# Performance work log

Measured on AMD Instinct MI355X. Metric: run time of the kernel, lower is better.

Reference implementation:

```python
import jax, jax.numpy as jnp
import numpy as np

H_DIM = 512
FF_DIM = 2048
N_HEAD = 4
N_BLOCK = 3
N_TOKEN = 128
B, S = 8, 1024
LN_EPS = 1e-5


def _layernorm(x, g, b):
    mu = jnp.mean(x, axis=-1, keepdims=True)
    var = jnp.mean(jnp.square(x - mu), axis=-1, keepdims=True)
    return (x - mu) * jax.lax.rsqrt(var + LN_EPS) * g + b


def setup_inputs() -> dict:
    key = jax.random.key(0)
    ks = jax.random.split(key, 20)
    sc = 0.02
    inp = {
        'input_ids': jax.random.randint(ks[0], (B, S), 0, N_TOKEN, dtype=jnp.int32),
        'attention_mask': jnp.ones((B, S), dtype=jnp.int32),
        'emb': jax.random.uniform(ks[1], (N_TOKEN, H_DIM), dtype=jnp.float32),
        'wq': jax.random.normal(ks[2], (N_BLOCK, N_HEAD, H_DIM, H_DIM), dtype=jnp.float32) * sc,
        'wk': jax.random.normal(ks[3], (N_BLOCK, N_HEAD, H_DIM, H_DIM), dtype=jnp.float32) * sc,
        'wv': jax.random.normal(ks[4], (N_BLOCK, N_HEAD, H_DIM, H_DIM), dtype=jnp.float32) * sc,
        'wo_w': jax.random.normal(ks[5], (N_BLOCK, N_HEAD * H_DIM, H_DIM), dtype=jnp.float32) * sc,
        'wo_b': jnp.zeros((N_BLOCK, H_DIM), dtype=jnp.float32),
        'ln1_g': jnp.ones((N_BLOCK, H_DIM), dtype=jnp.float32),
        'ln1_b': jnp.zeros((N_BLOCK, H_DIM), dtype=jnp.float32),
        'ff1_w': jax.random.normal(ks[6], (N_BLOCK, FF_DIM, H_DIM), dtype=jnp.float32) * sc,
        'ff1_b': jnp.zeros((N_BLOCK, FF_DIM), dtype=jnp.float32),
        'ff2_w': jax.random.normal(ks[7], (N_BLOCK, H_DIM, FF_DIM), dtype=jnp.float32) * sc,
        'ff2_b': jnp.zeros((N_BLOCK, H_DIM), dtype=jnp.float32),
        'ln2_g': jnp.ones((N_BLOCK, H_DIM), dtype=jnp.float32),
        'ln2_b': jnp.zeros((N_BLOCK, H_DIM), dtype=jnp.float32),
        'lm_w': jax.random.normal(ks[8], (H_DIM, N_TOKEN), dtype=jnp.float32) * sc,
    }
    return inp


def reference(emb, wq, wk, wv, wo_w, wo_b, ln1_g, ln1_b, ff1_w, ff1_b,
              ff2_w, ff2_b, ln2_g, ln2_b, lm_w, input_ids, attention_mask):
    mask_f = attention_mask.astype(jnp.float32)          # [B,S]
    valid = attention_mask != 0                          # [B,S]

    # Embedding lookup
    x = emb[input_ids]                                   # [B,S,H]

    # Positional encoding: positions assigned sequentially to valid tokens;
    # both even and odd feature slots get the SAME sin value (per source).
    pos = jnp.cumsum(mask_f, axis=-1) - 1.0              # [B,S]
    div = jnp.exp(jnp.arange(0, H_DIM, 2, dtype=jnp.float32) * (-jnp.log(10000.0) / H_DIM))  # [H/2]
    s = jnp.sin(pos[..., None] * div)                    # [B,S,H/2]
    pos_enc = jnp.repeat(s, 2, axis=-1) * mask_f[..., None]
    x = x + pos_enc

    # Allowed attention: causal (key <= query) AND query valid AND key valid
    rows = jnp.arange(S)
    causal = rows[None, :, None] >= rows[None, None, :]  # [1,S,S] (query>=key)
    allowed = causal & valid[:, :, None] & valid[:, None, :]  # [B,S,S]
    neg_inf = jnp.float32(-jnp.inf)
    scale = jnp.sqrt(jnp.float32(H_DIM))

    for l in range(N_BLOCK):
        # Per-head full-width attention (each head uses full H_DIM)
        q = jnp.einsum('bsh,nhd->bnsd', x, wq[l])
        k = jnp.einsum('bsh,nhd->bnsd', x, wk[l])
        v = jnp.einsum('bsh,nhd->bnsd', x, wv[l])
        scores = jnp.einsum('bnsd,bntd->bnst', q, k) / scale      # [B,N,S,S]
        scores = jnp.where(allowed[:, None], scores, neg_inf)
        att = jax.nn.softmax(scores, axis=-1)
        att = jnp.where(jnp.isnan(att), 0.0, att)                  # NaN rows -> 0
        o = jnp.einsum('bnst,bntd->bnsd', att, v)                  # [B,N,S,H]
        o = jnp.transpose(o, (0, 2, 1, 3)).reshape(B, S, N_HEAD * H_DIM)
        mh = o @ wo_w[l] + wo_b[l]
        x = _layernorm(x + mh, ln1_g[l], ln1_b[l])
        # Conv1d with kernel 1 == pointwise linear
        ff = jax.nn.relu(jnp.einsum('bsh,fh->bsf', x, ff1_w[l]) + ff1_b[l])
        ff = jnp.einsum('bsf,hf->bsh', ff, ff2_w[l]) + ff2_b[l]
        x = _layernorm(x + ff, ln2_g[l], ln2_b[l])

    return x @ lm_w                                       # [B,S,N_TOKEN]
```

## Files before the change

kernel.cpp:

```cpp
#include <hip/hip_runtime.h>
#include <hip/hip_bf16.h>

#define S_LEN 1024
#define BATCH 8
#define HD 512
#define FFD 2048
#define NHEAD 4
#define NBLK 3
#define NTOK 128

typedef __bf16 bf16_t;
typedef __bf16 bf16x4_t __attribute__((ext_vector_type(4)));
typedef __bf16 bf16x8_t __attribute__((ext_vector_type(8)));
typedef float f32x4_t __attribute__((ext_vector_type(4)));

typedef __attribute__((address_space(3))) uint32_t lds_u32;
typedef __attribute__((address_space(1))) uint32_t glb_u32;

template<int NI>
__device__ __forceinline__ void ldsread(const bf16_t* __restrict__ buf, int row0,
                                        int fr, int fg, int sw, bf16x8_t (&dst)[NI][2]) {
  #pragma unroll
  for (int i = 0; i < NI; ++i)
    #pragma unroll
    for (int ks = 0; ks < 2; ++ks)
      dst[i][ks] = *(const bf16x8_t*)&buf[(row0 + i*16 + fr)*64 + (((ks*4 + fg) ^ sw) << 3)];
}

template<int IB, int JB>
__device__ __forceinline__ void mquad(f32x4_t (&acc)[8][4],
                                      const bf16x8_t (&af)[4][2], const bf16x8_t (&bf)[2][2]) {
  #pragma unroll
  for (int ks = 0; ks < 2; ++ks)
    #pragma unroll
    for (int i = 0; i < 4; ++i)
      #pragma unroll
      for (int j = 0; j < 2; ++j)
        acc[IB+i][JB+j] = __builtin_amdgcn_mfma_f32_16x16x32_bf16(af[i][ks], bf[j][ks], acc[IB+i][JB+j], 0, 0, 0);
}

template<bool OUT_BF16, bool BIAS, bool RELU, bool CSKIP, bool CKLIM>
__global__ __launch_bounds__(512, 2)
void gemm256_kernel(const bf16_t* __restrict__ A,
                    const bf16_t* __restrict__ Bt,
                    const float* __restrict__ bias,
                    void* __restrict__ Cv,
                    int M, int N, int K,
                    int lda, int ldb, int ldc,
                    long long sA, long long sB, long long sBias,
                    int zshift, long long sC_hi, long long sC_lo,
                    int msub_shift, long long msub_stride,
                    float alpha)
{
  const int zb = blockIdx.z;
  const int m0 = blockIdx.x * 256;
  const int n0 = blockIdx.y * 256;
  if (CSKIP && n0 > m0 + 255) return;
  int kend = K;
  if (CKLIM) { int ke = m0 + 256; kend = ke < K ? ke : K; }
  const int nt = kend >> 6;

  const bf16_t* Az = A + (long long)zb * sA;
  const bf16_t* Bz = Bt + (long long)zb * sB;
  const long long coff = ((long long)(zb >> zshift)) * sC_hi
                       + ((long long)(zb & ((1 << zshift) - 1))) * sC_lo;

  __shared__ __align__(16) bf16_t As[2][256 * 64];
  __shared__ __align__(16) bf16_t Bs[2][256 * 64];

  const int tid = threadIdx.x;
  const int lane = tid & 63;
  const int w = tid >> 6;
  const int wm = (w >> 2) * 128;
  const int wn = (w & 3) * 64;
  const int fr = lane & 15;
  const int fg = lane >> 4;
  const int sw = fr & 7;

  const int srow = tid >> 3;
  const int scol8 = tid & 7;
  const int gswz = ((scol8 ^ (srow & 7)) << 3);

  f32x4_t acc[8][4];
  #pragma unroll
  for (int i = 0; i < 8; ++i)
    #pragma unroll
    for (int j = 0; j < 4; ++j)
      acc[i][j] = (f32x4_t){0.f, 0.f, 0.f, 0.f};

  const bf16_t* gA0 = Az + (long long)(m0 + srow) * lda + gswz;
  const bf16_t* gB0 = Bz + (long long)(n0 + srow) * ldb + gswz;

  auto stage_half = [&](int buf, int kt, int h) {
    if (h < 2) {
      const bf16_t* g = gA0 + (long long)(h * 128) * lda + (kt << 6);
      bf16_t* l = &As[buf][(h*128 + srow) * 64 + (scol8 << 3)];
      __builtin_amdgcn_global_load_lds((const glb_u32*)g, (lds_u32*)l, 16, 0, 0);
      __builtin_amdgcn_global_load_lds((const glb_u32*)(g + 64LL*lda), (lds_u32*)(l + 64*64), 16, 0, 0);
    } else {
      const int hh = h - 2;
      const bf16_t* g = gB0 + (long long)(hh * 128) * ldb + (kt << 6);
      bf16_t* l = &Bs[buf][(hh*128 + srow) * 64 + (scol8 << 3)];
      __builtin_amdgcn_global_load_lds((const glb_u32*)g, (lds_u32*)l, 16, 0, 0);
      __builtin_amdgcn_global_load_lds((const glb_u32*)(g + 64LL*ldb), (lds_u32*)(l + 64*64), 16, 0, 0);
    }
  };

  stage_half(0, 0, 0); stage_half(0, 0, 1); stage_half(0, 0, 2); stage_half(0, 0, 3);
  if (nt > 1) { stage_half(1, 1, 0); stage_half(1, 1, 1); }
  if (nt > 1) asm volatile("s_waitcnt vmcnt(4)" ::: "memory");
  else        asm volatile("s_waitcnt vmcnt(0)" ::: "memory");
  __builtin_amdgcn_s_barrier();
  __builtin_amdgcn_sched_barrier(0);

  for (int t = 0; t < nt; ++t) {
    const int cur = t & 1;
    const bf16_t* Ac = &As[cur][0];
    const bf16_t* Bc = &Bs[cur][0];
    bf16x8_t a0[4][2], a1[4][2], b0[2][2], b1[2][2];

    ldsread<4>(Ac, wm, fr, fg, sw, a0);
    ldsread<2>(Bc, wn, fr, fg, sw, b0);
    if (t + 1 < nt) stage_half(cur ^ 1, t + 1, 2);
    mquad<0, 0>(acc, a0, b0);
    ldsread<4>(Ac, wm + 64, fr, fg, sw, a1);
    ldsread<2>(Bc, wn + 32, fr, fg, sw, b1);
    if (t + 1 < nt) stage_half(cur ^ 1, t + 1, 3);
    mquad<4, 2>(acc, a1, b1);

    __builtin_amdgcn_s_barrier();
    __builtin_amdgcn_sched_barrier(0);

    if (t + 2 < nt) stage_half(cur, t + 2, 0);
    mquad<0, 2>(acc, a0, b1);
    if (t + 2 < nt) {
      stage_half(cur, t + 2, 1);
      asm volatile("s_waitcnt vmcnt(4)" ::: "memory");
    } else {
      asm volatile("s_waitcnt vmcnt(0)" ::: "memory");
    }
    mquad<4, 0>(acc, a1, b0);

    __builtin_amdgcn_s_barrier();
    __builtin_amdgcn_sched_barrier(0);
  }

  #pragma unroll
  for (int i = 0; i < 8; ++i) {
    #pragma unroll
    for (int e = 0; e < 4; ++e) {
      const int row = m0 + wm + i*16 + fg*4 + e;
      const long long ro = coff
        + ((long long)(row >> msub_shift)) * msub_stride
        + (long long)(row & ((1 << msub_shift) - 1)) * (long long)ldc;
      #pragma unroll
      for (int j = 0; j < 4; ++j) {
        const int col = n0 + wn + j*16 + fr;
        float v = acc[i][j][e] * alpha;
        if (BIAS) v += bias[(long long)zb * sBias + col];
        if (RELU) v = v > 0.f ? v : 0.f;
        if (OUT_BF16) ((bf16_t*)Cv)[ro + col] = (bf16_t)v;
        else          ((float*)Cv)[ro + col]  = v;
      }
    }
  }
}

template<bool OUT_BF16, bool BIAS, bool RELU, bool CSKIP, bool CKLIM>
__global__ __launch_bounds__(256, 4)
void gemm_bt_kernel(const bf16_t* __restrict__ A,
                    const bf16_t* __restrict__ Bt,
                    const float* __restrict__ bias,
                    void* __restrict__ Cv,
                    int M, int N, int K,
                    int lda, int ldb, int ldc,
                    long long sA, long long sB, long long sBias,
                    int zshift, long long sC_hi, long long sC_lo,
                    int msub_shift, long long msub_stride,
                    float alpha)
{
  const int zb = blockIdx.z;
  const int m0 = blockIdx.x * 128;
  const int n0 = blockIdx.y * 128;
  if (CSKIP && n0 > m0 + 127) return;
  int kend = K;
  if (CKLIM) { int ke = m0 + 128; kend = ke < K ? ke : K; }

  const bf16_t* Az = A + (long long)zb * sA;
  const bf16_t* Bz = Bt + (long long)zb * sB;
  const long long coff = ((long long)(zb >> zshift)) * sC_hi
                       + ((long long)(zb & ((1 << zshift) - 1))) * sC_lo;

  __shared__ __align__(16) bf16_t As[128 * 64];
  __shared__ __align__(16) bf16_t Bs[128 * 64];

  const int tid = threadIdx.x;
  const int wv = tid >> 6;
  const int lane = tid & 63;
  const int wm = (wv >> 1) * 64;
  const int wn = (wv & 1) * 64;
  const int fr = lane & 15;
  const int fg = lane >> 4;
  const int sw = fr & 7;

  f32x4_t acc[4][4];
  #pragma unroll
  for (int i = 0; i < 4; ++i)
    #pragma unroll
    for (int j = 0; j < 4; ++j)
      acc[i][j] = (f32x4_t){0.f, 0.f, 0.f, 0.f};

  const bf16_t* ga = Az + (long long)(m0 + (wv << 5) + (lane >> 3)) * lda
                   + (((lane & 7) ^ (lane >> 3)) << 3);
  const bf16_t* gb = Bz + (long long)(n0 + (wv << 5) + (lane >> 3)) * ldb
                   + (((lane & 7) ^ (lane >> 3)) << 3);

  for (int k0 = 0; k0 < kend; k0 += 64) {
    #pragma unroll
    for (int s = 0; s < 4; ++s) {
      __builtin_amdgcn_global_load_lds(
        (const glb_u32*)(ga + (long long)s * 8 * lda + k0),
        (lds_u32*)(As + (wv * 4 + s) * 512), 16, 0, 0);
      __builtin_amdgcn_global_load_lds(
        (const glb_u32*)(gb + (long long)s * 8 * ldb + k0),
        (lds_u32*)(Bs + (wv * 4 + s) * 512), 16, 0, 0);
    }
    __syncthreads();
    #pragma unroll
    for (int kc = 0; kc < 2; ++kc) {
      const int ca = ((kc * 4 + fg) ^ sw) << 3;
      bf16x8_t af[4], bfr[4];
      #pragma unroll
      for (int i = 0; i < 4; ++i)
        af[i] = *(const bf16x8_t*)&As[(wm + i*16 + fr) * 64 + ca];
      #pragma unroll
      for (int j = 0; j < 4; ++j)
        bfr[j] = *(const bf16x8_t*)&Bs[(wn + j*16 + fr) * 64 + ca];
      #pragma unroll
      for (int i = 0; i < 4; ++i)
        #pragma unroll
        for (int j = 0; j < 4; ++j)
          acc[i][j] = __builtin_amdgcn_mfma_f32_16x16x32_bf16(af[i], bfr[j], acc[i][j], 0, 0, 0);
    }
    __syncthreads();
  }

  #pragma unroll
  for (int i = 0; i < 4; ++i) {
    #pragma unroll
    for (int e = 0; e < 4; ++e) {
      const int row = m0 + wm + i*16 + fg*4 + e;
      const long long ro = coff
        + ((long long)(row >> msub_shift)) * msub_stride
        + (long long)(row & ((1 << msub_shift) - 1)) * (long long)ldc;
      #pragma unroll
      for (int j = 0; j < 4; ++j) {
        const int col = n0 + wn + j*16 + fr;
        float v = acc[i][j][e] * alpha;
        if (BIAS) v += bias[(long long)zb * sBias + col];
        if (RELU) v = v > 0.f ? v : 0.f;
        if (OUT_BF16) ((bf16_t*)Cv)[ro + col] = (bf16_t)v;
        else          ((float*)Cv)[ro + col]  = v;
      }
    }
  }
}

template<typename TIN>
__global__ void transpose_kernel(const TIN* __restrict__ in, bf16_t* __restrict__ out,
                                 int R, int C, long long sIn, long long sOut)
{
  __shared__ float tile[32][33];
  const long long zi = (long long)blockIdx.z * sIn;
  const long long zo = (long long)blockIdx.z * sOut;
  const int c0 = blockIdx.x * 32, r0 = blockIdx.y * 32;
  const int tx = threadIdx.x, ty = threadIdx.y;
  #pragma unroll
  for (int i = 0; i < 4; ++i) {
    int r = r0 + ty + i*8;
    tile[ty + i*8][tx] = (float)in[zi + (long long)r * C + c0 + tx];
  }
  __syncthreads();
  #pragma unroll
  for (int i = 0; i < 4; ++i) {
    int c = c0 + ty + i*8;
    out[zo + (long long)c * R + r0 + tx] = (bf16_t)tile[tx][ty + i*8];
  }
}

__global__ void qkvT_kernel(const float* __restrict__ wq, const float* __restrict__ wk,
                            const float* __restrict__ wv, bf16_t* __restrict__ out, int layer)
{
  __shared__ float tile[32][33];
  const int z = blockIdx.z, op = z >> 2, h = z & 3;
  const float* src = (op == 0 ? wq : op == 1 ? wk : wv)
                   + ((long long)layer * NHEAD + h) * HD * HD;
  bf16_t* dst = out + (long long)z * HD * HD;
  const int c0 = blockIdx.x * 32, r0 = blockIdx.y * 32;
  const int tx = threadIdx.x, ty = threadIdx.y;
  #pragma unroll
  for (int i = 0; i < 4; ++i)
    tile[ty + i*8][tx] = src[(long long)(r0 + ty + i*8) * HD + c0 + tx];
  __syncthreads();
  #pragma unroll
  for (int i = 0; i < 4; ++i)
    dst[(long long)(c0 + ty + i*8) * HD + r0 + tx] = (bf16_t)tile[tx][ty + i*8];
}

__global__ void convert2_kernel(const float* __restrict__ a, const float* __restrict__ b,
                                bf16_t* __restrict__ out, long long n)
{
  long long i = (long long)blockIdx.x * blockDim.x + threadIdx.x;
  long long stride = (long long)gridDim.x * blockDim.x;
  for (; i < 2*n; i += stride)
    out[i] = (bf16_t)(i < n ? a[i] : b[i - n]);
}

__global__ void fill_kernel(float* __restrict__ out, long long n, float v)
{
  long long i = (long long)blockIdx.x * blockDim.x + threadIdx.x;
  long long stride = (long long)gridDim.x * blockDim.x;
  for (; i < n; i += stride) out[i] = v;
}

__global__ void pos_kernel(const int* __restrict__ mask, float* __restrict__ pos)
{
  __shared__ float scn[S_LEN];
  const int b = blockIdx.x, t = threadIdx.x;
  scn[t] = (float)(mask[b * S_LEN + t] != 0);
  __syncthreads();
  for (int off = 1; off < S_LEN; off <<= 1) {
    float add = (t >= off) ? scn[t - off] : 0.f;
    __syncthreads();
    scn[t] += add;
    __syncthreads();
  }
  pos[b * S_LEN + t] = scn[t] - 1.0f;
}

__global__ void embed_kernel(const int* __restrict__ ids, const int* __restrict__ mask,
                             const float* __restrict__ pos, const float* __restrict__ emb,
                             float* __restrict__ x, bf16_t* __restrict__ xb)
{
  const int idx = blockIdx.x * 256 + threadIdx.x;
  const int i = idx & 255;
  const int bs = idx >> 8;
  const int id = ids[bs];
  const float m = (float)(mask[bs] != 0);
  const float p = pos[bs];
  const float dv = __expf(-(float)(2 * i) * (9.210340371976184f / (float)HD));
  const float sv = __sinf(p * dv) * m;
  const float e0 = emb[id * HD + 2*i], e1 = emb[id * HD + 2*i + 1];
  const float x0 = e0 + sv, x1 = e1 + sv;
  x[(long long)bs * HD + 2*i]     = x0;
  x[(long long)bs * HD + 2*i + 1] = x1;
  xb[(long long)bs * HD + 2*i]     = (bf16_t)x0;
  xb[(long long)bs * HD + 2*i + 1] = (bf16_t)x1;
}

__global__ void softmax_kernel(bf16_t* __restrict__ scP,
                               const int* __restrict__ mask, int pair0)
{
  const int lane = threadIdx.x & 63;
  const int s = blockIdx.x * 4 + (threadIdx.x >> 6);
  const int pz = blockIdx.y;
  const int b = (pair0 + pz) >> 2;
  bf16_t* row = scP + ((long long)pz * S_LEN + s) * S_LEN;
  const int t0 = lane * 16;

  bf16x8_t r0 = *(const bf16x8_t*)&row[t0];
  bf16x8_t r1 = *(const bf16x8_t*)&row[t0 + 8];
  int4 m4[4];
  #pragma unroll
  for (int q = 0; q < 4; ++q) m4[q] = *(const int4*)&mask[b * S_LEN + t0 + q*4];
  const int* mm = (const int*)m4;

  float v[16]; bool ok[16];
  #pragma unroll
  for (int j = 0; j < 16; ++j) {
    const int t = t0 + j;
    ok[j] = (t <= s) && (mm[j] != 0);
    float raw = (j < 8) ? (float)r0[j] : (float)r1[j - 8];
    v[j] = ok[j] ? raw : -INFINITY;
  }
  float mx = v[0];
  #pragma unroll
  for (int j = 1; j < 16; ++j) mx = fmaxf(mx, v[j]);
  #pragma unroll
  for (int o = 32; o; o >>= 1) mx = fmaxf(mx, __shfl_xor(mx, o));

  float e[16]; float sum = 0.f;
  #pragma unroll
  for (int j = 0; j < 16; ++j) { e[j] = ok[j] ? __expf(v[j] - mx) : 0.f; sum += e[j]; }
  #pragma unroll
  for (int o = 32; o; o >>= 1) sum += __shfl_xor(sum, o);

  const bool qvalid = mask[b * S_LEN + s] != 0;
  const float inv = (qvalid && sum > 0.f) ? 1.f / sum : 0.f;
  bf16x8_t o0, o1;
  #pragma unroll
  for (int j = 0; j < 8; ++j) { o0[j] = (bf16_t)(e[j] * inv); o1[j] = (bf16_t)(e[j+8] * inv); }
  *(bf16x8_t*)&row[t0] = o0;
  *(bf16x8_t*)&row[t0 + 8] = o1;
}

__global__ void ln_kernel(float* __restrict__ x, const float* __restrict__ tparts,
                          int ns, long long pstride,
                          const float* __restrict__ bias,
                          const float* __restrict__ g, const float* __restrict__ b,
                          bf16_t* __restrict__ xb)
{
  const int lane = threadIdx.x & 63;
  const long long row = (long long)blockIdx.x * 4 + (threadIdx.x >> 6);
  const int e0 = lane * 8;
  const long long base = row * HD + e0;

  float4 xa = *(const float4*)&x[base];
  float4 xc = *(const float4*)&x[base + 4];
  float4 ba = *(const float4*)&bias[e0];
  float4 bc = *(const float4*)&bias[e0 + 4];
  float v[8] = {xa.x+ba.x, xa.y+ba.y, xa.z+ba.z, xa.w+ba.w,
                xc.x+bc.x, xc.y+bc.y, xc.z+bc.z, xc.w+bc.w};
  for (int i = 0; i < ns; ++i) {
    float4 p0 = *(const float4*)&tparts[i*pstride + base];
    float4 p1 = *(const float4*)&tparts[i*pstride + base + 4];
    v[0]+=p0.x; v[1]+=p0.y; v[2]+=p0.z; v[3]+=p0.w;
    v[4]+=p1.x; v[5]+=p1.y; v[6]+=p1.z; v[7]+=p1.w;
  }
  float s = 0.f;
  #pragma unroll
  for (int j = 0; j < 8; ++j) s += v[j];
  #pragma unroll
  for (int o = 32; o; o >>= 1) s += __shfl_xor(s, o);
  const float mu = s * (1.f / (float)HD);
  float q = 0.f;
  #pragma unroll
  for (int j = 0; j < 8; ++j) { v[j] -= mu; q += v[j]*v[j]; }
  #pragma unroll
  for (int o = 32; o; o >>= 1) q += __shfl_xor(q, o);
  const float inv = rsqrtf(q * (1.f / (float)HD) + 1e-5f);

  float4 ga4 = *(const float4*)&g[e0];
  float4 gc4 = *(const float4*)&g[e0 + 4];
  float4 bb4 = *(const float4*)&b[e0];
  float4 bd4 = *(const float4*)&b[e0 + 4];
  float y[8] = {v[0]*inv*ga4.x+bb4.x, v[1]*inv*ga4.y+bb4.y, v[2]*inv*ga4.z+bb4.z, v[3]*inv*ga4.w+bb4.w,
                v[4]*inv*gc4.x+bd4.x, v[5]*inv*gc4.y+bd4.y, v[6]*inv*gc4.z+bd4.z, v[7]*inv*gc4.w+bd4.w};
  *(float4*)&x[base]     = (float4){y[0],y[1],y[2],y[3]};
  *(float4*)&x[base + 4] = (float4){y[4],y[5],y[6],y[7]};
  bf16x8_t yb;
  #pragma unroll
  for (int j = 0; j < 8; ++j) yb[j] = (bf16_t)y[j];
  *(bf16x8_t*)&xb[base] = yb;
}

extern "C" void kernel_launch(void* const* d_in, const int* in_sizes, int n_in,
                              void* d_out, int out_size, void* d_ws, size_t ws_size,
                              hipStream_t stream)
{
  (void)in_sizes; (void)n_in;
  const int*   ids   = (const int*)d_in[0];
  const int*   amask = (const int*)d_in[1];
  const float* emb   = (const float*)d_in[2];
  const float* wq    = (const float*)d_in[3];
  const float* wk    = (const float*)d_in[4];
  const float* wv    = (const float*)d_in[5];
  const float* wo_w  = (const float*)d_in[6];
  const float* wo_b  = (const float*)d_in[7];
  const float* ln1_g = (const float*)d_in[8];
  const float* ln1_b = (const float*)d_in[9];
  const float* ff1_w = (const float*)d_in[10];
  const float* ff1_b = (const float*)d_in[11];
  const float* ff2_w = (const float*)d_in[12];
  const float* ff2_b = (const float*)d_in[13];
  const float* ln2_g = (const float*)d_in[14];
  const float* ln2_b = (const float*)d_in[15];
  const float* lm_w  = (const float*)d_in[16];

  const long long MROW = (long long)BATCH * S_LEN;
  const size_t MBc = 1ull << 20;
  char* p = (char*)d_ws;
  auto alloc = [&](size_t bytes) { char* r = p; p += (bytes + 255) & ~(size_t)255; return r; };

  float*  x     = (float*) alloc(MROW * HD * 4);
  bf16_t* xb    = (bf16_t*)alloc(MROW * HD * 2);
  bf16_t* ob    = (bf16_t*)alloc(MROW * (NHEAD*HD) * 2);
  bf16_t* wqkvT = (bf16_t*)alloc(12LL * HD * HD * 2);
  bf16_t* woT   = (bf16_t*)alloc((long long)HD * FFD * 2);
  bf16_t* wff1  = (bf16_t*)alloc((long long)FFD * HD * 2);
  bf16_t* wff2  = (bf16_t*)alloc((long long)HD * FFD * 2);
  bf16_t* lmT   = (bf16_t*)alloc((long long)NTOK * HD * 2);
  float*  pos   = (float*) alloc(MROW * 4);

  const size_t used = (size_t)(p - (char*)d_ws);
  const size_t rem  = ws_size > used ? ws_size - used : 0;

  int P = 0, SK = 2;
  if      (rem >= 160 * MBc) { P = 32; SK = 4; }
  else if (rem >= 64 * MBc)  { P = 8;  SK = 2; }
  if (P == 0) {
    fill_kernel<<<1024, 256, 0, stream>>>((float*)d_out, (long long)out_size,
                                          (float)(ws_size >> 20));
    return;
  }

  char* A = p;
  const long long pairE = (long long)S_LEN * HD;
  bf16_t* qc  = (bf16_t*)A;
  bf16_t* kc  = qc  + (long long)P * pairE;
  bf16_t* vTc = kc  + (long long)P * pairE;
  bf16_t* scb = vTc + (long long)P * pairE;
  float*  tmp = (float*)A;
  bf16_t* ffb = (bf16_t*)(A + (size_t)SK * 16 * MBc);

  const dim3 tb(32, 8);
  transpose_kernel<float><<<dim3(4,16,1), tb, 0, stream>>>(lm_w, lmT, HD, NTOK, 0, 0);
  pos_kernel<<<BATCH, S_LEN, 0, stream>>>(amask, pos);
  embed_kernel<<<8192, 256, 0, stream>>>(ids, amask, pos, emb, x, xb);

  const int nch = 32 / P;
  const int bpc = P / NHEAD;

  for (int l = 0; l < NBLK; ++l) {
    qkvT_kernel<<<dim3(16,16,12), tb, 0, stream>>>(wq, wk, wv, wqkvT, l);
    transpose_kernel<float><<<dim3(16,64,1), tb, 0, stream>>>(
      wo_w + (long long)l*FFD*HD, woT, FFD, HD, 0, 0);
    convert2_kernel<<<2048, 256, 0, stream>>>(
      ff1_w + (long long)l*FFD*HD, ff2_w + (long long)l*HD*FFD, wff1, (long long)FFD*HD);

    for (int c = 0; c < nch; ++c) {
      const int b0 = c * bpc;
      const int pair0 = b0 * NHEAD;
      const int Mch = bpc * S_LEN;

      gemm256_kernel<true,false,false,false,false><<<dim3(Mch/256,2,8),512,0,stream>>>(
        xb + (long long)b0*S_LEN*HD, wqkvT, nullptr, qc, Mch, HD, HD, HD, HD, HD,
        0, (long long)HD*HD, 0,
        2, (long long)P*pairE, (long long)S_LEN*HD,
        10, (long long)NHEAD*S_LEN*HD, 1.f);

      gemm256_kernel<true,false,false,false,false><<<dim3(8,4,bpc),512,0,stream>>>(
        wqkvT + 8LL*HD*HD, xb + (long long)b0*S_LEN*HD, nullptr, vTc,
        2048, S_LEN, HD, HD, HD, S_LEN,
        0, (long long)S_LEN*HD, 0,
        0, (long long)NHEAD*HD*S_LEN, 0,
        9, (long long)HD*S_LEN, 1.f);

      gemm256_kernel<true,false,false,true,false><<<dim3(4,4,P),512,0,stream>>>(
        qc, kc, nullptr, scb,
        S_LEN, S_LEN, HD, HD, HD, S_LEN,
        (long long)S_LEN*HD, (long long)S_LEN*HD, 0,
        30, 0, (long long)S_LEN*S_LEN,
        30, 0, 0.044194173824159216f);
      softmax_kernel<<<dim3(S_LEN/4,P),256,0,stream>>>(scb, amask, pair0);
      gemm256_kernel<true,false,false,false,true><<<dim3(4,2,P),512,0,stream>>>(
        scb, vTc, nullptr,
        ob + (long long)b0*S_LEN*(NHEAD*HD),
        S_LEN, HD, S_LEN, S_LEN, S_LEN, NHEAD*HD,
        (long long)S_LEN*S_LEN, (long long)HD*S_LEN, 0,
        2, (long long)S_LEN*NHEAD*HD, HD,
        30, 0, 1.f);
    }

    gemm256_kernel<false,false,false,false,false><<<dim3(32,2,SK),512,0,stream>>>(
      ob, woT, nullptr, tmp,
      (int)MROW, HD, (NHEAD*HD)/SK, NHEAD*HD, NHEAD*HD, HD,
      (NHEAD*HD)/SK, (NHEAD*HD)/SK, 0,
      0, (long long)MROW*HD, 0,
      30, 0, 1.f);
    ln_kernel<<<2048,256,0,stream>>>(x, tmp, SK, (long long)MROW*HD,
                                     wo_b + l*HD, ln1_g + l*HD, ln1_b + l*HD, xb);

    gemm256_kernel<true,true,true,false,false><<<dim3(32,8,1),512,0,stream>>>(
      xb, wff1, ff1_b + l*FFD, ffb,
      (int)MROW, FFD, HD, HD, HD, FFD,
      0, 0, 0, 30, 0, 0, 30, 0, 1.f);
    gemm256_kernel<false,false,false,false,false><<<dim3(32,2,SK),512,0,stream>>>(
      ffb, wff2, nullptr, tmp,
      (int)MROW, HD, FFD/SK, FFD, FFD, HD,
      FFD/SK, FFD/SK, 0,
      0, (long long)MROW*HD, 0,
      30, 0, 1.f);
    ln_kernel<<<2048,256,0,stream>>>(x, tmp, SK, (long long)MROW*HD,
                                     ff2_b + l*HD, ln2_g + l*HD, ln2_b + l*HD, xb);
  }

  gemm_bt_kernel<false,false,false,false,false><<<dim3(64,1,1),256,0,stream>>>(
    xb, lmT, nullptr, (float*)d_out,
    (int)MROW, NTOK, HD, HD, HD, NTOK,
    0, 0, 0, 30, 0, 0, 30, 0, 1.f);
}
```

Measured before the change: 899.4 us.

## Fold Wq·Wkᵀ into one matrix, drop K projection, launch triangular score tiles

```diff
diff --git a/kernel.cpp b/kernel.cpp
--- a/kernel.cpp
+++ b/kernel.cpp
@@ -39,7 +39,7 @@
         acc[IB+i][JB+j] = __builtin_amdgcn_mfma_f32_16x16x32_bf16(af[i][ks], bf[j][ks], acc[IB+i][JB+j], 0, 0, 0);
 }
 
-template<bool OUT_BF16, bool BIAS, bool RELU, bool CSKIP, bool CKLIM>
+template<bool OUT_BF16, bool BIAS, bool RELU, bool TRI, bool CKLIM>
 __global__ __launch_bounds__(512, 2)
 void gemm256_kernel(const bf16_t* __restrict__ A,
                     const bf16_t* __restrict__ Bt,
@@ -47,21 +47,30 @@
                     void* __restrict__ Cv,
                     int M, int N, int K,
                     int lda, int ldb, int ldc,
-                    long long sA, long long sB, long long sBias,
+                    long long sA, long long sB, int bshift, long long sBias,
                     int zshift, long long sC_hi, long long sC_lo,
                     int msub_shift, long long msub_stride,
                     float alpha)
 {
   const int zb = blockIdx.z;
-  const int m0 = blockIdx.x * 256;
-  const int n0 = blockIdx.y * 256;
-  if (CSKIP && n0 > m0 + 255) return;
+  int m0, n0;
+  if (TRI) {
+    const int idx = blockIdx.x;
+    int mi = (int)((sqrtf(8.f * idx + 1.f) - 1.f) * 0.5f);
+    while ((mi + 1) * (mi + 2) / 2 <= idx) ++mi;
+    while (mi * (mi + 1) / 2 > idx) --mi;
+    m0 = mi * 256;
+    n0 = (idx - mi * (mi + 1) / 2) * 256;
+  } else {
+    m0 = blockIdx.x * 256;
+    n0 = blockIdx.y * 256;
+  }
   int kend = K;
   if (CKLIM) { int ke = m0 + 256; kend = ke < K ? ke : K; }
   const int nt = kend >> 6;
 
   const bf16_t* Az = A + (long long)zb * sA;
-  const bf16_t* Bz = Bt + (long long)zb * sB;
+  const bf16_t* Bz = Bt + (long long)(zb >> bshift) * sB;
   const long long coff = ((long long)(zb >> zshift)) * sC_hi
                        + ((long long)(zb & ((1 << zshift) - 1))) * sC_lo;
 
@@ -167,7 +176,7 @@
 }
 
 template<bool OUT_BF16, bool BIAS, bool RELU, bool CSKIP, bool CKLIM>
-__global__ __launch_bounds__(256, 4)
+__global__ __launch_bounds__(256, 2)
 void gemm_bt_kernel(const bf16_t* __restrict__ A,
                     const bf16_t* __restrict__ Bt,
                     const float* __restrict__ bias,
@@ -286,25 +295,6 @@
     int c = c0 + ty + i*8;
     out[zo + (long long)c * R + r0 + tx] = (bf16_t)tile[tx][ty + i*8];
   }
-}
-
-__global__ void qkvT_kernel(const float* __restrict__ wq, const float* __restrict__ wk,
-                            const float* __restrict__ wv, bf16_t* __restrict__ out, int layer)
-{
-  __shared__ float tile[32][33];
-  const int z = blockIdx.z, op = z >> 2, h = z & 3;
-  const float* src = (op == 0 ? wq : op == 1 ? wk : wv)
-                   + ((long long)layer * NHEAD + h) * HD * HD;
-  bf16_t* dst = out + (long long)z * HD * HD;
-  const int c0 = blockIdx.x * 32, r0 = blockIdx.y * 32;
-  const int tx = threadIdx.x, ty = threadIdx.y;
-  #pragma unroll
-  for (int i = 0; i < 4; ++i)
-    tile[ty + i*8][tx] = src[(long long)(r0 + ty + i*8) * HD + c0 + tx];
-  __syncthreads();
-  #pragma unroll
-  for (int i = 0; i < 4; ++i)
-    dst[(long long)(c0 + ty + i*8) * HD + r0 + tx] = (bf16_t)tile[tx][ty + i*8];
 }
 
 __global__ void convert2_kernel(const float* __restrict__ a, const float* __restrict__ b,
@@ -485,7 +475,9 @@
   float*  x     = (float*) alloc(MROW * HD * 4);
   bf16_t* xb    = (bf16_t*)alloc(MROW * HD * 2);
   bf16_t* ob    = (bf16_t*)alloc(MROW * (NHEAD*HD) * 2);
-  bf16_t* wqkvT = (bf16_t*)alloc(12LL * HD * HD * 2);
+  bf16_t* wqkb  = (bf16_t*)alloc(8LL * HD * HD * 2);
+  bf16_t* wvT   = (bf16_t*)alloc(4LL * HD * HD * 2);
+  bf16_t* Gt    = (bf16_t*)alloc(4LL * HD * HD * 2);
   bf16_t* woT   = (bf16_t*)alloc((long long)HD * FFD * 2);
   bf16_t* wff1  = (bf16_t*)alloc((long long)FFD * HD * 2);
   bf16_t* wff2  = (bf16_t*)alloc((long long)HD * FFD * 2);
@@ -496,7 +488,7 @@
   const size_t rem  = ws_size > used ? ws_size - used : 0;
 
   int P = 0, SK = 2;
-  if      (rem >= 160 * MBc) { P = 32; SK = 4; }
+  if      (rem >= 128 * MBc) { P = 32; SK = 4; }
   else if (rem >= 64 * MBc)  { P = 8;  SK = 2; }
   if (P == 0) {
     fill_kernel<<<1024, 256, 0, stream>>>((float*)d_out, (long long)out_size,
@@ -507,8 +499,7 @@
   char* A = p;
   const long long pairE = (long long)S_LEN * HD;
   bf16_t* qc  = (bf16_t*)A;
-  bf16_t* kc  = qc  + (long long)P * pairE;
-  bf16_t* vTc = kc  + (long long)P * pairE;
+  bf16_t* vTc = qc  + (long long)P * pairE;
   bf16_t* scb = vTc + (long long)P * pairE;
   float*  tmp = (float*)A;
   bf16_t* ffb = (bf16_t*)(A + (size_t)SK * 16 * MBc);
@@ -522,38 +513,47 @@
   const int bpc = P / NHEAD;
 
   for (int l = 0; l < NBLK; ++l) {
-    qkvT_kernel<<<dim3(16,16,12), tb, 0, stream>>>(wq, wk, wv, wqkvT, l);
+    convert2_kernel<<<2048, 256, 0, stream>>>(
+      wq + (long long)l*NHEAD*HD*HD, wk + (long long)l*NHEAD*HD*HD, wqkb, 4LL*HD*HD);
+    transpose_kernel<float><<<dim3(16,16,4), tb, 0, stream>>>(
+      wv + (long long)l*NHEAD*HD*HD, wvT, HD, HD, (long long)HD*HD, (long long)HD*HD);
     transpose_kernel<float><<<dim3(16,64,1), tb, 0, stream>>>(
       wo_w + (long long)l*FFD*HD, woT, FFD, HD, 0, 0);
     convert2_kernel<<<2048, 256, 0, stream>>>(
       ff1_w + (long long)l*FFD*HD, ff2_w + (long long)l*HD*FFD, wff1, (long long)FFD*HD);
+    gemm_bt_kernel<true,false,false,false,false><<<dim3(4,4,4),256,0,stream>>>(
+      wqkb + 4LL*HD*HD, wqkb, nullptr, Gt,
+      HD, HD, HD, HD, HD, HD,
+      (long long)HD*HD, (long long)HD*HD, 0,
+      30, 0, (long long)HD*HD,
+      30, 0, 1.f);
 
     for (int c = 0; c < nch; ++c) {
       const int b0 = c * bpc;
       const int pair0 = b0 * NHEAD;
       const int Mch = bpc * S_LEN;
 
-      gemm256_kernel<true,false,false,false,false><<<dim3(Mch/256,2,8),512,0,stream>>>(
-        xb + (long long)b0*S_LEN*HD, wqkvT, nullptr, qc, Mch, HD, HD, HD, HD, HD,
-        0, (long long)HD*HD, 0,
-        2, (long long)P*pairE, (long long)S_LEN*HD,
-        10, (long long)NHEAD*S_LEN*HD, 1.f);
+      gemm256_kernel<true,false,false,false,false><<<dim3(Mch/256,2,4),512,0,stream>>>(
+        xb + (long long)b0*S_LEN*HD, Gt, nullptr, qc, Mch, HD, HD, HD, HD, HD,
+        0, (long long)HD*HD, 0, 0,
+        2, 0, pairE,
+        10, (long long)NHEAD*pairE, 1.f);
 
       gemm256_kernel<true,false,false,false,false><<<dim3(8,4,bpc),512,0,stream>>>(
-        wqkvT + 8LL*HD*HD, xb + (long long)b0*S_LEN*HD, nullptr, vTc,
+        wvT, xb + (long long)b0*S_LEN*HD, nullptr, vTc,
         2048, S_LEN, HD, HD, HD, S_LEN,
-        0, (long long)S_LEN*HD, 0,
+        0, (long long)S_LEN*HD, 0, 0,
         0, (long long)NHEAD*HD*S_LEN, 0,
         9, (long long)HD*S_LEN, 1.f);
 
-      gemm256_kernel<true,false,false,true,false><<<dim3(4,4,P),512,0,stream>>>(
-        qc, kc, nullptr, scb,
+      gemm256_kernel<true,false,false,true,false><<<dim3(10,1,P),512,0,stream>>>(
+        qc, xb + (long long)b0*S_LEN*HD, nullptr, scb,
         S_LEN, S_LEN, HD, HD, HD, S_LEN,
-        (long long)S_LEN*HD, (long long)S_LEN*HD, 0,
+        pairE, (long long)S_LEN*HD, 2, 0,
         30, 0, (long long)S_LEN*S_LEN,
         30, 0, 0.044194173824159216f);
       softmax_kernel<<<dim3(S_LEN/4,P),256,0,stream>>>(scb, amask, pair0);
-      gemm256_kernel<true,false,false,false,true><<<dim3(4,2,P),512,0,stream>>>(
+      gemm_bt_kernel<true,false,false,false,true><<<dim3(8,4,P),256,0,stream>>>(
         scb, vTc, nullptr,
         ob + (long long)b0*S_LEN*(NHEAD*HD),
         S_LEN, HD, S_LEN, S_LEN, S_LEN, NHEAD*HD,
@@ -565,7 +565,7 @@
     gemm256_kernel<false,false,false,false,false><<<dim3(32,2,SK),512,0,stream>>>(
       ob, woT, nullptr, tmp,
       (int)MROW, HD, (NHEAD*HD)/SK, NHEAD*HD, NHEAD*HD, HD,
-      (NHEAD*HD)/SK, (NHEAD*HD)/SK, 0,
+      (NHEAD*HD)/SK, (NHEAD*HD)/SK, 0, 0,
       0, (long long)MROW*HD, 0,
       30, 0, 1.f);
     ln_kernel<<<2048,256,0,stream>>>(x, tmp, SK, (long long)MROW*HD,
@@ -574,11 +574,11 @@
     gemm256_kernel<true,true,true,false,false><<<dim3(32,8,1),512,0,stream>>>(
       xb, wff1, ff1_b + l*FFD, ffb,
       (int)MROW, FFD, HD, HD, HD, FFD,
-      0, 0, 0, 30, 0, 0, 30, 0, 1.f);
+      0, 0, 0, 0, 30, 0, 0, 30, 0, 1.f);
     gemm256_kernel<false,false,false,false,false><<<dim3(32,2,SK),512,0,stream>>>(
       ffb, wff2, nullptr, tmp,
       (int)MROW, HD, FFD/SK, FFD, FFD, HD,
-      FFD/SK, FFD/SK, 0,
+      FFD/SK, FFD/SK, 0, 0,
       0, (long long)MROW*HD, 0,
       30, 0, 1.f);
     ln_kernel<<<2048,256,0,stream>>>(x, tmp, SK, (long long)MROW*HD,
```

Result: no change. 902.4 us (+0.3%).
